# Kernel tuning notes

Measured on AMD Instinct MI355X. Metric: run time of the kernel, lower is better.

Reference implementation:

```python
import jax, jax.numpy as jnp
import numpy as np
import math

N, FB, D, H, HD, L, K = 512, 256, 64, 128, 4, 4, 100
# note: H=num_heads=4, HD=head_dim=128 -> inner dim H*HD = 512
H, HD = 4, 128
HHD = H * HD
EPS = 1e-5


def mish(x):
    return x * jnp.tanh(jax.nn.softplus(x))


def layer_norm(x, g, b):
    mu = jnp.mean(x, axis=-1, keepdims=True)
    var = jnp.var(x, axis=-1, keepdims=True)
    return (x - mu) * jax.lax.rsqrt(var + EPS) * g + b


def setup_inputs() -> dict:
    key = jax.random.key(0)
    ks = jax.random.split(key, 16)
    def lin(k, fan_in, shape):
        return jax.random.normal(k, shape, jnp.float32) / np.sqrt(fan_in)
    return {
        "node_features": jax.random.normal(ks[0], (N, FB), jnp.float32),
        "amds": jax.random.uniform(ks[1], (N, K), jnp.float32),
        "emb_W": lin(ks[2], FB, (FB, D)),
        "emb_b": jnp.zeros((D,), jnp.float32),
        "bias_emb_W": lin(ks[3], K, (K, D)),
        "bias_emb_b": jnp.zeros((D,), jnp.float32),
        "ln1_g": jnp.ones((D,), jnp.float32),
        "ln1_b": jnp.zeros((D,), jnp.float32),
        "ln2_g": jnp.ones((D,), jnp.float32),
        "ln2_b": jnp.zeros((D,), jnp.float32),
        "qkv_W": lin(ks[4], D, (L, D, 3 * HHD)),
        "qkv_b": jnp.zeros((L, 3 * HHD), jnp.float32),
        "diff_W": lin(ks[5], D, (L, D, HHD)),
        "diff_b": jnp.zeros((L, HHD), jnp.float32),
        "o_W": lin(ks[6], HHD, (L, HHD, D)),
        "o_b": jnp.zeros((L, D), jnp.float32),
        "bout_W": lin(ks[7], HHD, (L, HHD, D)),
        "bout_b": jnp.zeros((L, D), jnp.float32),
        "out_W": lin(ks[8], D, (D, 1)),
        "out_b": jnp.zeros((1,), jnp.float32),
    }


def reference(node_features, amds, emb_W, emb_b, bias_emb_W, bias_emb_b,
              ln1_g, ln1_b, ln2_g, ln2_b, qkv_W, qkv_b, diff_W, diff_b,
              o_W, o_b, bout_W, bout_b, out_W, out_b):
    h = node_features @ emb_W + emb_b                     # [N, D]
    b0 = amds @ bias_emb_W + bias_emb_b                   # [N, D]
    bias = b0[None, :, :] - b0[:, None, :]                # [N, N, D]
    x = layer_norm(h, ln1_g, ln1_b)
    scale = 1.0 / math.sqrt(HD)
    for l in range(L):
        qkv = (x @ qkv_W[l] + qkv_b[l]).reshape(N, H, 3 * HD)
        q, k, v = jnp.split(qkv, 3, axis=-1)              # each [N, H, HD]
        be = mish(bias @ diff_W[l] + diff_b[l])           # [N, N, H*HD]
        diffs = jnp.linalg.norm(be.reshape(N, N, H, HD), axis=-1)  # [N, N, H]
        diffs = jnp.transpose(diffs, (2, 0, 1))           # [H, N, N]
        logits = jnp.einsum('nhd,mhd->hnm', q, k) * scale + diffs
        attn = jax.nn.softmax(logits, axis=-1)            # [H, N, N]
        vals = jnp.einsum('hnm,mhd->nhd', attn, v).reshape(N, HHD)
        temp_x = vals @ o_W[l] + o_b[l]                   # [N, D]
        bias = mish(be @ bout_W[l] + bout_b[l])           # [N, N, D]
        x = layer_norm(x + temp_x, ln2_g, ln2_b)
    return x @ out_W + out_b                              # [N, 1]
```

## Files before the change

kernel.cpp:

```cpp
#include <hip/hip_runtime.h>
#include <hip/hip_bf16.h>
#include <hip/hip_fp16.h>
#include <cmath>


namespace {

constexpr int kN   = 512;
constexpr int kD   = 64;
constexpr int kH   = 4;
constexpr int kHD  = 128;
constexpr int kHHD = 512;
constexpr int kFB  = 256;
constexpr int kK   = 100;
constexpr float kEps   = 1e-5f;
constexpr float kScale = 0.08838834764831845f;

typedef unsigned short u16;
typedef unsigned int u32;
typedef short bf16x8 __attribute__((ext_vector_type(8)));
typedef _Float16 f16x8 __attribute__((ext_vector_type(8)));
typedef float f32x4 __attribute__((ext_vector_type(4)));
typedef float f32x2 __attribute__((ext_vector_type(2)));

__device__ __forceinline__ f32x2 mish2(f32x2 x) {
    float e0 = __expf(x[0]);
    float e1 = __expf(x[1]);
    f32x2 e  = {e0, e1};
    f32x2 n2 = __builtin_elementwise_fma(e, e + 2.0f, (f32x2)(2.0f));
    f32x2 r  = {__builtin_amdgcn_rcpf(n2[0]), __builtin_amdgcn_rcpf(n2[1])};
    return __builtin_elementwise_fma(x + x, -r, x);
}

__device__ __forceinline__ u32 pkh(float a, float b) {
    union { __half2 h; u32 u; } cv;
    cv.h = __float22half2_rn(make_float2(a, b));
    return cv.u;
}
__device__ __forceinline__ f16x8 mkh8(u32 a, u32 b, u32 c, u32 d) {
    union { u32 w[4]; f16x8 v; } cv;
    cv.w[0] = a; cv.w[1] = b; cv.w[2] = c; cv.w[3] = d;
    return cv.v;
}
__device__ __forceinline__ u16 f16_bits(float f) {
    union { __half h; u16 u; } cv;
    cv.h = __float2half(f);
    return cv.u;
}

__device__ __forceinline__ float dot4(float4 a, float4 b, float acc) {
    acc = fmaf(a.x, b.x, acc);
    acc = fmaf(a.y, b.y, acc);
    acc = fmaf(a.z, b.z, acc);
    acc = fmaf(a.w, b.w, acc);
    return acc;
}
__device__ __forceinline__ float4 fma4(float s, float4 v, float4 d) {
    d.x = fmaf(s, v.x, d.x);
    d.y = fmaf(s, v.y, d.y);
    d.z = fmaf(s, v.z, d.z);
    d.w = fmaf(s, v.w, d.w);
    return d;
}

__global__ __launch_bounds__(64) void embed_kernel(
    const float* __restrict__ nf, const float* __restrict__ amds,
    const float* __restrict__ emb_W, const float* __restrict__ emb_b,
    const float* __restrict__ bemb_W, const float* __restrict__ bemb_b,
    const float* __restrict__ ln1_g, const float* __restrict__ ln1_b,
    float* __restrict__ x, float* __restrict__ b0)
{
    const int n = blockIdx.x;
    const int d = threadIdx.x;
    __shared__ float s_row[kFB];
    #pragma unroll
    for (int r = 0; r < kFB / kD; ++r) s_row[r * kD + d] = nf[n * kFB + r * kD + d];
    __syncthreads();
    float acc = emb_b[d];
    for (int k = 0; k < kFB; ++k) acc = fmaf(s_row[k], emb_W[k * kD + d], acc);
    float mu = acc;
    #pragma unroll
    for (int off = 32; off > 0; off >>= 1) mu += __shfl_xor(mu, off);
    mu *= (1.0f / kD);
    float dv = acc - mu;
    float var = dv * dv;
    #pragma unroll
    for (int off = 32; off > 0; off >>= 1) var += __shfl_xor(var, off);
    var *= (1.0f / kD);
    x[n * kD + d] = dv * rsqrtf(var + kEps) * ln1_g[d] + ln1_b[d];
    __syncthreads();
    s_row[d] = amds[n * kK + d];
    if (d < kK - kD) s_row[kD + d] = amds[n * kK + kD + d];
    __syncthreads();
    float bacc = bemb_b[d];
    for (int k = 0; k < kK; ++k) bacc = fmaf(s_row[k], bemb_W[k * kD + d], bacc);
    b0[n * kD + d] = bacc;
}

__global__ __launch_bounds__(256) void prep_weights_kernel(
    const float* __restrict__ diff_W, const float* __restrict__ bout_W,
    u16* __restrict__ dWt, u16* __restrict__ boutWt)
{
    int gid = blockIdx.x * 256 + threadIdx.x;
    if (gid < 4 * 32768) {
        int e = gid;
        int l = e >> 15;
        int r = e & 32767;
        int k = r >> 9;
        int n = r & 511;
        dWt[l * 32768 + n * 64 + k] = f16_bits(diff_W[e]);
    } else {
        int e = gid - 4 * 32768;
        int l = e >> 15;
        int r = e & 32767;
        int k = r >> 6;
        int d = r & 63;
        boutWt[l * 32768 + d * 512 + k] = f16_bits(bout_W[e]);
    }
}

__global__ __launch_bounds__(256, 2) void bias_layer_mfma(
    u16* __restrict__ bias,
    const u16* __restrict__ dWt, const u16* __restrict__ boutWt,
    const float* __restrict__ diff_b, const float* __restrict__ bout_b,
    const float* __restrict__ b0, float* __restrict__ diffs,
    const float* __restrict__ x, const float* __restrict__ qW,
    const float* __restrict__ qb, float* __restrict__ qkv,
    int last, int first)
{
    __shared__ u16 s_w[2][4096];
    __shared__ float s_db[kHHD];
    __shared__ float s_x[2 * kD];

    const int t    = threadIdx.x;
    const int w    = t >> 6;
    const int lane = t & 63;
    const int q    = lane >> 4;
    const int c    = lane & 15;
    const int pb   = blockIdx.x * 128 + w * 32;

    const int sb_bc  = t >> 3;
    const int sb_kb  = t & 7;
    const int sr     = ((sb_bc >> 2) & 1) * 16 + ((sb_bc >> 3) << 2) + (sb_bc & 3);
    const int w1_dst = sr * 64 + (sb_kb ^ (sr & 7)) * 8;
    const int sb_d   = t >> 2;
    const int sb_k2  = t & 3;
    const int w2_dst = 2048 + sb_d * 32 + (sb_k2 ^ ((sb_d >> 1) & 3)) * 8;
    const u16* g_w1 = dWt + sb_bc * 64 + sb_kb * 8;
    const u16* g_w2 = boutWt + sb_d * 512 + sb_k2 * 8;

    f16x8 Bf[2][2];
    if (first) {
        const int ii = pb >> 9;
        const float* bi = b0 + ii * kD;
        #pragma unroll
        for (int mt = 0; mt < 2; ++mt) {
            const int jj = (pb & 511) + mt * 16 + c;
            const float* bj = b0 + jj * kD;
            #pragma unroll
            for (int s = 0; s < 2; ++s) {
                const int d0 = s * 32 + q * 8;
                float4 a0 = *(const float4*)(bj + d0);
                float4 a1v = *(const float4*)(bj + d0 + 4);
                float4 c0 = *(const float4*)(bi + d0);
                float4 c1v = *(const float4*)(bi + d0 + 4);
                Bf[mt][s] = mkh8(pkh(a0.x - c0.x, a0.y - c0.y),
                                 pkh(a0.z - c0.z, a0.w - c0.w),
                                 pkh(a1v.x - c1v.x, a1v.y - c1v.y),
                                 pkh(a1v.z - c1v.z, a1v.w - c1v.w));
            }
        }
    } else {
        #pragma unroll
        for (int mt = 0; mt < 2; ++mt) {
            #pragma unroll
            for (int s = 0; s < 2; ++s) {
                Bf[mt][s] = *(const f16x8*)(bias + (long)(pb + mt * 16 + c) * kD + s * 32 + q * 8);
            }
        }
    }

    {
        bf16x8 r0 = *(const bf16x8*)g_w1;
        bf16x8 r1 = *(const bf16x8*)g_w2;
        *(bf16x8*)&s_w[0][w1_dst] = r0;
        *(bf16x8*)&s_w[0][w2_dst] = r1;
        s_db[t] = diff_b[t];
        s_db[256 + t] = diff_b[256 + t];
        if (t < 2 * kD) s_x[t] = x[(blockIdx.x >> 3) * 2 * kD + t];
    }
    __syncthreads();

    if (t < 192) {
        const int row0 = (blockIdx.x >> 3) * 2;
        const int cc = (blockIdx.x & 7) * 192 + t;
        float a0 = qb[cc];
        float a1 = a0;
        #pragma unroll 8
        for (int k = 0; k < kD; ++k) {
            float wv = qW[k * (3 * kHHD) + cc];
            a0 = fmaf(s_x[k], wv, a0);
            a1 = fmaf(s_x[kD + k], wv, a1);
        }
        qkv[row0 * (3 * kHHD) + cc] = a0;
        qkv[(row0 + 1) * (3 * kHHD) + cc] = a1;
    }

    f32x4 acc2[2][4];
    #pragma unroll
    for (int mt = 0; mt < 2; ++mt)
        #pragma unroll
        for (int dg = 0; dg < 4; ++dg) acc2[mt][dg] = (f32x4)0.0f;
    f32x2 psum2[2][4];
    #pragma unroll
    for (int mt = 0; mt < 2; ++mt)
        #pragma unroll
        for (int h = 0; h < 4; ++h) psum2[mt][h] = (f32x2)0.0f;

    const int sw1 = c & 7;
    const int sw2 = (c >> 1) & 3;
    int cur = 0;

    for (int g2 = 0; g2 < 16; ++g2) {
        bf16x8 r0, r1;
        if (g2 < 15) {
            r0 = *(const bf16x8*)(g_w1 + (g2 + 1) * 2048);
            r1 = *(const bf16x8*)(g_w2 + (g2 + 1) * 32);
        }

        const f32x4 db4l = *(const f32x4*)&s_db[g2 * 32 + q * 8];
        const f32x4 db4h = *(const f32x4*)&s_db[g2 * 32 + q * 8 + 4];
        f32x4 a1[2][2];
        #pragma unroll
        for (int mt = 0; mt < 2; ++mt) {
            a1[mt][0] = db4l;
            a1[mt][1] = db4h;
        }
        const u16* w1 = &s_w[cur][0];
        #pragma unroll
        for (int u = 0; u < 2; ++u) {
            int row = (u * 16 + c) * 64;
            int o0 = row + ((0 + q) ^ sw1) * 8;
            int o1 = row + ((4 + q) ^ sw1) * 8;
            f16x8 A0 = *(const f16x8*)(w1 + o0);
            f16x8 A1 = *(const f16x8*)(w1 + o1);
            #pragma unroll
            for (int mt = 0; mt < 2; ++mt) {
                a1[mt][u] = __builtin_amdgcn_mfma_f32_16x16x32_f16(A0, Bf[mt][0], a1[mt][u], 0, 0, 0);
                a1[mt][u] = __builtin_amdgcn_mfma_f32_16x16x32_f16(A1, Bf[mt][1], a1[mt][u], 0, 0, 0);
            }
        }

        const int hd = g2 >> 2;
        f16x8 A2[2];
        #pragma unroll
        for (int mt = 0; mt < 2; ++mt) {
            u32 p[2][2];
            #pragma unroll
            for (int u = 0; u < 2; ++u) {
                f32x2 xlo = {a1[mt][u][0], a1[mt][u][1]};
                f32x2 xhi = {a1[mt][u][2], a1[mt][u][3]};
                f32x2 vlo = mish2(xlo);
                f32x2 vhi = mish2(xhi);
                psum2[mt][hd] = __builtin_elementwise_fma(vlo, vlo, psum2[mt][hd]);
                psum2[mt][hd] = __builtin_elementwise_fma(vhi, vhi, psum2[mt][hd]);
                p[u][0] = pkh(vlo[0], vlo[1]);
                p[u][1] = pkh(vhi[0], vhi[1]);
            }
            A2[mt] = mkh8(p[0][0], p[0][1], p[1][0], p[1][1]);
        }

        if (!last) {
            const u16* w2 = &s_w[cur][2048];
            const int kb2 = (q ^ sw2) * 8;
            #pragma unroll
            for (int dg = 0; dg < 4; ++dg) {
                int bo = dg * 512 + c * 32 + kb2;
                f16x8 Wf = *(const f16x8*)(w2 + bo);
                #pragma unroll
                for (int mt = 0; mt < 2; ++mt) {
                    acc2[mt][dg] = __builtin_amdgcn_mfma_f32_16x16x32_f16(A2[mt], Wf, acc2[mt][dg], 0, 0, 0);
                }
            }
        }

        if (g2 < 15) {
            int nb = cur ^ 1;
            *(bf16x8*)&s_w[nb][w1_dst] = r0;
            *(bf16x8*)&s_w[nb][w2_dst] = r1;
            __syncthreads();
            cur = nb;
        }
    }

    if (!last) {
        #pragma unroll
        for (int mt = 0; mt < 2; ++mt) {
            #pragma unroll
            for (int dg = 0; dg < 4; ++dg) {
                float bb = bout_b[dg * 16 + c];
                f32x2 bb2 = {bb, bb};
                f32x2 vlo = mish2(f32x2{acc2[mt][dg][0], acc2[mt][dg][1]} + bb2);
                f32x2 vhi = mish2(f32x2{acc2[mt][dg][2], acc2[mt][dg][3]} + bb2);
                const long rbase = (long)(pb + mt * 16 + 4 * q);
                bias[(rbase + 0) * kD + dg * 16 + c] = f16_bits(vlo[0]);
                bias[(rbase + 1) * kD + dg * 16 + c] = f16_bits(vlo[1]);
                bias[(rbase + 2) * kD + dg * 16 + c] = f16_bits(vhi[0]);
                bias[(rbase + 3) * kD + dg * 16 + c] = f16_bits(vhi[1]);
            }
        }
    }
    const int i  = blockIdx.x >> 2;
    const int jb = (blockIdx.x & 3) * 128 + w * 32;
    #pragma unroll
    for (int mt = 0; mt < 2; ++mt) {
        float psum[4];
        #pragma unroll
        for (int h = 0; h < 4; ++h) {
            psum[h] = psum2[mt][h][0] + psum2[mt][h][1];
            psum[h] += __shfl_xor(psum[h], 16);
            psum[h] += __shfl_xor(psum[h], 32);
        }
        float sv = (q == 0) ? psum[0] : (q == 1) ? psum[1]
                 : (q == 2) ? psum[2] : psum[3];
        diffs[q * (kN * kN) + i * kN + jb + mt * 16 + c] = sqrtf(sv);
    }
}

__global__ __launch_bounds__(512) void flash_attn_kernel(
    const float* __restrict__ qkv, const float* __restrict__ diffs,
    float* __restrict__ part, float* __restrict__ ml)
{
    __shared__ float s_a[32 * 132];
    __shared__ float s_b[128 * 36];

    const int t  = threadIdx.x;
    const int tx = t & 31;
    const int ty = t >> 5;
    const int r0 = ty * 2;
    const int n0 = blockIdx.x * 32;
    const int mq = blockIdx.y;
    const int h  = blockIdx.z;
    const int m0 = mq * 128;

    #pragma unroll
    for (int rep = 0; rep < 2; ++rep) {
        int f = rep * 512 + t;
        int row = f >> 5;
        int c4  = f & 31;
        *(float4*)&s_a[row * 132 + c4 * 4] =
            *(const float4*)&qkv[(n0 + row) * (3 * kHHD) + h * 384 + c4 * 4];
    }

    float acc[2][4];
    #pragma unroll
    for (int i = 0; i < 2; ++i)
        #pragma unroll
        for (int cc = 0; cc < 4; ++cc) acc[i][cc] = 0.0f;

    for (int db = 0; db < 4; ++db) {
        __syncthreads();
        #pragma unroll
        for (int rep = 0; rep < 2; ++rep) {
            int f = rep * 512 + t;
            int col = f >> 3;
            int c4  = f & 7;
            *(float4*)&s_b[col * 36 + c4 * 4] =
                *(const float4*)&qkv[(m0 + col) * (3 * kHHD) + h * 384 + 128 + db * 32 + c4 * 4];
        }
        __syncthreads();
        #pragma unroll
        for (int k4 = 0; k4 < 8; ++k4) {
            float4 a0 = *(const float4*)&s_a[(r0 + 0) * 132 + db * 32 + k4 * 4];
            float4 a1 = *(const float4*)&s_a[(r0 + 1) * 132 + db * 32 + k4 * 4];
            #pragma unroll
            for (int cc = 0; cc < 4; ++cc) {
                float4 b = *(const float4*)&s_b[(tx + 32 * cc) * 36 + k4 * 4];
                acc[0][cc] = dot4(a0, b, acc[0][cc]);
                acc[1][cc] = dot4(a1, b, acc[1][cc]);
            }
        }
    }

    float mr[2], lr[2];
    #pragma unroll
    for (int i = 0; i < 2; ++i) {
        const float* dro = diffs + h * (kN * kN) + (n0 + r0 + i) * kN + m0 + tx;
        #pragma unroll
        for (int cc = 0; cc < 4; ++cc)
            acc[i][cc] = fmaf(acc[i][cc], kScale, dro[32 * cc]);
        float m = fmaxf(fmaxf(acc[i][0], acc[i][1]), fmaxf(acc[i][2], acc[i][3]));
        #pragma unroll
        for (int off = 1; off < 32; off <<= 1) m = fmaxf(m, __shfl_xor(m, off));
        mr[i] = m;
        float l = 0.0f;
        #pragma unroll
        for (int cc = 0; cc < 4; ++cc) {
            float p = __expf(acc[i][cc] - m);
            acc[i][cc] = p;
            l += p;
        }
        #pragma unroll
        for (int off = 1; off < 32; off <<= 1) l += __shfl_xor(l, off);
        lr[i] = l;
    }

    __syncthreads();
    #pragma unroll
    for (int i = 0; i < 2; ++i) {
        #pragma unroll
        for (int cc = 0; cc < 4; ++cc)
            s_a[(r0 + i) * 132 + tx + 32 * cc] = acc[i][cc];
        if (tx == 0)
            *(float2*)&ml[((h * 4 + mq) * kN + n0 + r0 + i) * 2] = make_float2(mr[i], lr[i]);
    }

    float4 o0 = {0,0,0,0}, o1 = {0,0,0,0};
    for (int ms = 0; ms < 4; ++ms) {
        if (ms > 0) __syncthreads();
        #pragma unroll
        for (int rep = 0; rep < 2; ++rep) {
            int f = rep * 512 + t;
            int row = f >> 5;
            int c4  = f & 31;
            *(float4*)&s_b[row * 132 + c4 * 4] =
                *(const float4*)&qkv[(m0 + ms * 32 + row) * (3 * kHHD) + h * 384 + 256 + c4 * 4];
        }
        __syncthreads();
        #pragma unroll
        for (int k4 = 0; k4 < 8; ++k4) {
            float4 p0 = *(const float4*)&s_a[(r0 + 0) * 132 + ms * 32 + k4 * 4];
            float4 p1 = *(const float4*)&s_a[(r0 + 1) * 132 + ms * 32 + k4 * 4];
            #pragma unroll
            for (int u = 0; u < 4; ++u) {
                float4 v = *(const float4*)&s_b[(k4 * 4 + u) * 132 + tx * 4];
                float pu0 = (u == 0) ? p0.x : (u == 1) ? p0.y : (u == 2) ? p0.z : p0.w;
                float pu1 = (u == 0) ? p1.x : (u == 1) ? p1.y : (u == 2) ? p1.z : p1.w;
                o0 = fma4(pu0, v, o0);
                o1 = fma4(pu1, v, o1);
            }
        }
    }
    const int pbase = (h * 4 + mq) * (kN * kHD) + (n0 + r0) * kHD + 4 * tx;
    *(float4*)&part[pbase]       = o0;
    *(float4*)&part[pbase + kHD] = o1;
}

__global__ __launch_bounds__(256) void oproj_ln_kernel(
    const float* __restrict__ part, const float* __restrict__ ml,
    const float* __restrict__ o_W, const float* __restrict__ o_b,
    const float* __restrict__ g2, const float* __restrict__ b2,
    float* __restrict__ x,
    const float* __restrict__ out_W, const float* __restrict__ out_b,
    float* __restrict__ out, int dofinal)
{
    const int n = blockIdx.x;
    const int t = threadIdx.x;
    const int w = t >> 6;
    const int d = t & 63;
    __shared__ float s_v[kHHD];
    __shared__ float s_part[4][kD];
    #pragma unroll
    for (int r = 0; r < 2; ++r) {
        int j  = r * 256 + t;
        int h  = j >> 7;
        int dd = j & 127;
        float2 m_l[4];
        float M = -1e30f;
        #pragma unroll
        for (int q = 0; q < 4; ++q) {
            m_l[q] = *(const float2*)&ml[((h * 4 + q) * kN + n) * 2];
            M = fmaxf(M, m_l[q].x);
        }
        float L = 0.0f, wq[4];
        #pragma unroll
        for (int q = 0; q < 4; ++q) {
            wq[q] = __expf(m_l[q].x - M);
            L = fmaf(wq[q], m_l[q].y, L);
        }
        float sv = 0.0f;
        #pragma unroll
        for (int q = 0; q < 4; ++q) {
            sv = fmaf(wq[q], part[(h * 4 + q) * (kN * kHD) + n * kHD + dd], sv);
        }
        s_v[j] = sv / L;
    }
    __syncthreads();
    float acc = 0.0f;
    #pragma unroll 4
    for (int j = 0; j < 128; ++j)
        acc = fmaf(s_v[w * 128 + j], o_W[(w * 128 + j) * kD + d], acc);
    s_part[w][d] = acc;
    __syncthreads();
    if (t < kD) {
        float av = o_b[d] + ((s_part[0][d] + s_part[1][d]) + (s_part[2][d] + s_part[3][d]));
        float xv = x[n * kD + d] + av;
        float mu = xv;
        #pragma unroll
        for (int off = 32; off > 0; off >>= 1) mu += __shfl_xor(mu, off);
        mu *= (1.0f / kD);
        float dv = xv - mu;
        float var = dv * dv;
        #pragma unroll
        for (int off = 32; off > 0; off >>= 1) var += __shfl_xor(var, off);
        var *= (1.0f / kD);
        float xnew = dv * rsqrtf(var + kEps) * g2[d] + b2[d];
        x[n * kD + d] = xnew;
        if (dofinal) {
            float p = xnew * out_W[d];
            #pragma unroll
            for (int off = 32; off > 0; off >>= 1) p += __shfl_xor(p, off);
            if (d == 0) out[n] = p + out_b[0];
        }
    }
}

}

extern "C" void kernel_launch(void* const* d_in, const int* in_sizes, int n_in,
                              void* d_out, int out_size, void* d_ws, size_t ws_size,
                              hipStream_t stream)
{
    (void)in_sizes; (void)n_in; (void)out_size; (void)ws_size;

    const float* nf     = (const float*)d_in[0];
    const float* amds   = (const float*)d_in[1];
    const float* emb_W  = (const float*)d_in[2];
    const float* emb_b  = (const float*)d_in[3];
    const float* bemb_W = (const float*)d_in[4];
    const float* bemb_b = (const float*)d_in[5];
    const float* ln1_g  = (const float*)d_in[6];
    const float* ln1_b  = (const float*)d_in[7];
    const float* ln2_g  = (const float*)d_in[8];
    const float* ln2_b  = (const float*)d_in[9];
    const float* qkv_W  = (const float*)d_in[10];
    const float* qkv_b  = (const float*)d_in[11];
    const float* diff_W = (const float*)d_in[12];
    const float* diff_b = (const float*)d_in[13];
    const float* o_W    = (const float*)d_in[14];
    const float* o_b    = (const float*)d_in[15];
    const float* bout_W = (const float*)d_in[16];
    const float* bout_b = (const float*)d_in[17];
    const float* out_W  = (const float*)d_in[18];
    const float* out_b  = (const float*)d_in[19];

    float* ws = (float*)d_ws;
    float* ws_x      = ws;
    float* ws_b0     = ws_x + 32768;
    float* ws_qkv    = ws_b0 + 32768;
    float* ws_ml     = ws_qkv + 786432;
    float* ws_diffs  = ws_ml + 262144;
    float* ws_part   = ws_diffs + 1048576;
    u16*   ws_bias   = (u16*)(ws_part + 1048576);
    u16*   dWt       = ws_bias + 16777216;
    u16*   boutWt    = dWt + 131072;

    embed_kernel<<<kN, kD, 0, stream>>>(nf, amds, emb_W, emb_b, bemb_W, bemb_b,
                                        ln1_g, ln1_b, ws_x, ws_b0);
    prep_weights_kernel<<<(2 * 4 * 32768) / 256, 256, 0, stream>>>(
        diff_W, bout_W, dWt, boutWt);

    for (int l = 0; l < 4; ++l) {
        bias_layer_mfma<<<kN * kN / 128, 256, 0, stream>>>(
            ws_bias, dWt + l * 32768, boutWt + l * 32768,
            diff_b + l * kHHD, bout_b + l * kD, ws_b0, ws_diffs,
            ws_x, qkv_W + l * kD * (3 * kHHD), qkv_b + l * (3 * kHHD), ws_qkv,
            (l == 3) ? 1 : 0, (l == 0) ? 1 : 0);
        flash_attn_kernel<<<dim3(16, 4, kH), 512, 0, stream>>>(
            ws_qkv, ws_diffs, ws_part, ws_ml);
        oproj_ln_kernel<<<kN, 256, 0, stream>>>(
            ws_part, ws_ml, o_W + l * kHHD * kD, o_b + l * kD, ln2_g, ln2_b, ws_x,
            out_W, out_b, (float*)d_out, (l == 3) ? 1 : 0);
    }
}
```

Baseline: 474.8 us.

## Fuse attention combine, output projection and LayerNorm into next layer's bias kernel

For layers after the first, the bias/MFMA kernel now merges the flash-attention partials, applies the output projection and LayerNorm for its two rows, and feeds the result straight into the QKV projection. This drops three oproj_ln launches and the round trip of x through global memory between kernels. In exchange, each of the 8 blocks that share a row pair recomputes the combine and projection redundantly (only one writes x), and x is double-buffered to avoid read/write races. This adds prologue latency to the heavy bias kernel.

```diff
diff --git a/kernel.cpp b/kernel.cpp
--- a/kernel.cpp
+++ b/kernel.cpp
@@ -124,13 +124,19 @@
     const u16* __restrict__ dWt, const u16* __restrict__ boutWt,
     const float* __restrict__ diff_b, const float* __restrict__ bout_b,
     const float* __restrict__ b0, float* __restrict__ diffs,
-    const float* __restrict__ x, const float* __restrict__ qW,
-    const float* __restrict__ qb, float* __restrict__ qkv,
-    int last, int first)
+    const float* __restrict__ x_in, float* __restrict__ x_out,
+    const float* __restrict__ qW, const float* __restrict__ qb,
+    float* __restrict__ qkv,
+    const float* __restrict__ part, const float* __restrict__ ml,
+    const float* __restrict__ oW, const float* __restrict__ ob,
+    const float* __restrict__ g2ln, const float* __restrict__ b2ln,
+    int last, int first, int comb)
 {
     __shared__ u16 s_w[2][4096];
     __shared__ float s_db[kHHD];
     __shared__ float s_x[2 * kD];
+    __shared__ float s_v[2][kHHD];
+    __shared__ float s_part[4][kD];
 
     const int t    = threadIdx.x;
     const int w    = t >> 6;
@@ -138,6 +144,7 @@
     const int q    = lane >> 4;
     const int c    = lane & 15;
     const int pb   = blockIdx.x * 128 + w * 32;
+    const int n0r  = (blockIdx.x >> 3) * 2;
 
     const int sb_bc  = t >> 3;
     const int sb_kb  = t & 7;
@@ -187,12 +194,75 @@
         *(bf16x8*)&s_w[0][w2_dst] = r1;
         s_db[t] = diff_b[t];
         s_db[256 + t] = diff_b[256 + t];
-        if (t < 2 * kD) s_x[t] = x[(blockIdx.x >> 3) * 2 * kD + t];
-    }
-    __syncthreads();
+    }
+
+    if (comb) {
+        #pragma unroll
+        for (int p = t; p < 1024; p += 256) {
+            const int row = p >> 9;
+            const int j   = p & 511;
+            const int hh  = j >> 7;
+            const int dd  = j & 127;
+            const int n   = n0r + row;
+            float2 m_l[4];
+            float M = -1e30f;
+            #pragma unroll
+            for (int qq = 0; qq < 4; ++qq) {
+                m_l[qq] = *(const float2*)&ml[((hh * 4 + qq) * kN + n) * 2];
+                M = fmaxf(M, m_l[qq].x);
+            }
+            float L = 0.0f, wq[4];
+            #pragma unroll
+            for (int qq = 0; qq < 4; ++qq) {
+                wq[qq] = __expf(m_l[qq].x - M);
+                L = fmaf(wq[qq], m_l[qq].y, L);
+            }
+            float sv = 0.0f;
+            #pragma unroll
+            for (int qq = 0; qq < 4; ++qq)
+                sv = fmaf(wq[qq], part[(hh * 4 + qq) * (kN * kHD) + n * kHD + dd], sv);
+            s_v[row][j] = sv / L;
+        }
+        __syncthreads();
+        {
+            const int d = t & 63, row = w >> 1, half = w & 1;
+            float acc = 0.0f;
+            const float* vp = &s_v[row][half * 256];
+            const float* wp = oW + (half * 256) * kD + d;
+            #pragma unroll 4
+            for (int j = 0; j < 256; ++j)
+                acc = fmaf(vp[j], wp[j * kD], acc);
+            s_part[w][d] = acc;
+        }
+        __syncthreads();
+        {
+            const int d = t & 63;
+            if ((w & 1) == 0) {
+                const int r2 = w >> 1;
+                const int n = n0r + r2;
+                float av = ob[d] + (s_part[w][d] + s_part[w + 1][d]);
+                float xv = x_in[n * kD + d] + av;
+                float mu = xv;
+                #pragma unroll
+                for (int off = 32; off > 0; off >>= 1) mu += __shfl_xor(mu, off);
+                mu *= (1.0f / kD);
+                float dv = xv - mu;
+                float var = dv * dv;
+                #pragma unroll
+                for (int off = 32; off > 0; off >>= 1) var += __shfl_xor(var, off);
+                var *= (1.0f / kD);
+                float xnew = dv * rsqrtf(var + kEps) * g2ln[d] + b2ln[d];
+                s_x[r2 * kD + d] = xnew;
+                if ((blockIdx.x & 7) == 0) x_out[n * kD + d] = xnew;
+            }
+        }
+        __syncthreads();
+    } else {
+        if (t < 2 * kD) s_x[t] = x_in[n0r * kD + t];
+        __syncthreads();
+    }
 
     if (t < 192) {
-        const int row0 = (blockIdx.x >> 3) * 2;
         const int cc = (blockIdx.x & 7) * 192 + t;
         float a0 = qb[cc];
         float a1 = a0;
@@ -202,8 +272,8 @@
             a0 = fmaf(s_x[k], wv, a0);
             a1 = fmaf(s_x[kD + k], wv, a1);
         }
-        qkv[row0 * (3 * kHHD) + cc] = a0;
-        qkv[(row0 + 1) * (3 * kHHD) + cc] = a1;
+        qkv[n0r * (3 * kHHD) + cc] = a0;
+        qkv[(n0r + 1) * (3 * kHHD) + cc] = a1;
     }
 
     f32x4 acc2[2][4];
@@ -549,6 +619,7 @@
     float* ws_b0     = ws_x + 32768;
     float* ws_qkv    = ws_b0 + 32768;
     float* ws_ml     = ws_qkv + 786432;
+    float* ws_x2     = ws_ml + 131072;
     float* ws_diffs  = ws_ml + 262144;
     float* ws_part   = ws_diffs + 1048576;
     u16*   ws_bias   = (u16*)(ws_part + 1048576);
@@ -560,16 +631,23 @@
     prep_weights_kernel<<<(2 * 4 * 32768) / 256, 256, 0, stream>>>(
         diff_W, bout_W, dWt, boutWt);
 
+    float* xbuf[2] = {ws_x, ws_x2};
     for (int l = 0; l < 4; ++l) {
+        const float* xin = (l == 0) ? xbuf[0] : xbuf[(l + 1) & 1];
+        float* xout = xbuf[l & 1];
+        const int lprev = (l > 0) ? (l - 1) : 0;
         bias_layer_mfma<<<kN * kN / 128, 256, 0, stream>>>(
             ws_bias, dWt + l * 32768, boutWt + l * 32768,
             diff_b + l * kHHD, bout_b + l * kD, ws_b0, ws_diffs,
-            ws_x, qkv_W + l * kD * (3 * kHHD), qkv_b + l * (3 * kHHD), ws_qkv,
-            (l == 3) ? 1 : 0, (l == 0) ? 1 : 0);
+            xin, xout,
+            qkv_W + l * kD * (3 * kHHD), qkv_b + l * (3 * kHHD), ws_qkv,
+            ws_part, ws_ml, o_W + lprev * kHHD * kD, o_b + lprev * kD,
+            ln2_g, ln2_b,
+            (l == 3) ? 1 : 0, (l == 0) ? 1 : 0, (l > 0) ? 1 : 0);
         flash_attn_kernel<<<dim3(16, 4, kH), 512, 0, stream>>>(
             ws_qkv, ws_diffs, ws_part, ws_ml);
-        oproj_ln_kernel<<<kN, 256, 0, stream>>>(
-            ws_part, ws_ml, o_W + l * kHHD * kD, o_b + l * kD, ln2_g, ln2_b, ws_x,
-            out_W, out_b, (float*)d_out, (l == 3) ? 1 : 0);
-    }
-}
+    }
+    oproj_ln_kernel<<<kN, 256, 0, stream>>>(
+        ws_part, ws_ml, o_W + 3 * kHHD * kD, o_b + 3 * kD, ln2_g, ln2_b, xbuf[1],
+        out_W, out_b, (float*)d_out, 1);
+}
```

Result: slower. 546.6 us (+15.1%).
